# Optimization experiments

Measured on AMD Instinct MI355X. Metric: run time of the kernel, lower is better.

Reference implementation:

```python
import jax, jax.numpy as jnp
import numpy as np

B, N, NQ, D, H = 16, 1024, 1024, 512, 8
HD = D // H  # per-head kq dim and per-head v-output dim (64)


def setup_inputs() -> dict:
    key = jax.random.key(0)
    ks = jax.random.split(key, 7)
    s = 0.02  # small init like torch Linear default scale
    return {
        "x":   jax.random.normal(ks[0], (B, N, D), jnp.float32),
        "r":   jax.random.normal(ks[1], (B, N, D), jnp.float32),
        "x_q": jax.random.normal(ks[2], (B, NQ, D), jnp.float32),
        # per-head projection weights, torch Linear layout (out, in), stacked over heads
        "Wq": jax.random.normal(ks[3], (H, HD, D), jnp.float32) * s,
        "Wk": jax.random.normal(ks[4], (H, HD, D), jnp.float32) * s,
        "Wv": jax.random.normal(ks[5], (H, HD, D), jnp.float32) * s,  # applied AFTER attention
        "Wo": jax.random.normal(ks[6], (D, D), jnp.float32) * s,
    }


def reference(x, r, x_q, Wq, Wk, Wv, Wo):
    # AttentionAggregator.forward(x, r, x_q) -> MultiHeadAttention(q=x_q, k=x, v=r)
    qh = jnp.einsum('bnd,hed->bhne', x_q, Wq)            # (B,H,NQ,HD)
    kh = jnp.einsum('bmd,hed->bhme', x, Wk)              # (B,H,N,HD)
    scale = jnp.sqrt(jnp.float32(HD))                    # sqrt(d_k) with d_k = head_kq_dim_out
    scores = jnp.einsum('bhne,bhme->bhnm', qh, kh) / scale
    attn = jax.nn.softmax(scores, axis=-1)               # normalize=True path
    # NOTE: v (=r) is NOT projected before attention in the original module
    ctx = jnp.einsum('bhnm,bmd->bhnd', attn, r)          # (B,H,NQ,D)
    heads = jnp.einsum('bhnd,hed->bhne', ctx, Wv)        # (B,H,NQ,HD), per-head post-projection
    concat = heads.transpose(0, 2, 1, 3).reshape(B, NQ, H * HD)  # cat over heads, dim=-1
    return concat @ Wo.T                                 # head_o (post_process=True)
```

## Files before the change

kernel.cpp:

```cpp
#include <hip/hip_runtime.h>


#define B_  16
#define N_  1024
#define D_  512
#define H_  8

typedef short short8 __attribute__((ext_vector_type(8)));
typedef float f32x4 __attribute__((ext_vector_type(4)));
typedef unsigned short ushort;
typedef unsigned int uint;

__device__ __forceinline__ ushort bf16rne(float f) {
  uint u = __float_as_uint(f);
  u += 0x7FFFu + ((u >> 16) & 1u);
  return (ushort)(u >> 16);
}
__device__ __forceinline__ uint bf16pk(float lo, float hi) {
  return (uint)bf16rne(lo) | ((uint)bf16rne(hi) << 16);
}
__device__ __forceinline__ void gload_lds16(const void* g, void* l) {
  __builtin_amdgcn_global_load_lds(
      (const __attribute__((address_space(1))) uint*)g,
      (__attribute__((address_space(3))) uint*)l, 16, 0, 0);
}

__global__ __launch_bounds__(256) void cast_bf16_k(
    const float* __restrict__ s, ushort* __restrict__ d, long n, float scale)
{
  long i = ((long)blockIdx.x * 256 + threadIdx.x) * 8;
  if (i >= n) return;
  float4 v0 = *(const float4*)(s + i);
  float4 v1 = *(const float4*)(s + i + 4);
  uint4 o;
  o.x = bf16pk(v0.x * scale, v0.y * scale);
  o.y = bf16pk(v0.z * scale, v0.w * scale);
  o.z = bf16pk(v1.x * scale, v1.y * scale);
  o.w = bf16pk(v1.z * scale, v1.w * scale);
  *(uint4*)(d + i) = o;
}

template <typename OutT>
__global__ __launch_bounds__(256) void gemm_bt(
    const ushort* __restrict__ A, const ushort* __restrict__ W,
    OutT* __restrict__ C, int M, int N, int K)
{
  __shared__ __align__(16) ushort Al[128 * 64];
  __shared__ __align__(16) ushort Bl[128 * 64];
  const int t = threadIdx.x, lane = t & 63, w = t >> 6;
  const int g = lane >> 4, lr = lane & 15;
  const int wr = w >> 1, wc = w & 1;
  const long m0 = (long)blockIdx.y * 128, n0 = (long)blockIdx.x * 128;

  f32x4 acc[4][4] = {};

  for (int k0 = 0; k0 < K; k0 += 64) {
    __syncthreads();
    #pragma unroll
    for (int u = 0; u < 4; ++u) {
      const int a = t * 16 + u * 4096;
      const int row = a >> 7, ch = (a >> 4) & 7;
      const int kk = k0 + ((ch ^ (row & 7)) << 3);
      gload_lds16(A + (m0 + row) * K + kk, (char*)Al + a);
      gload_lds16(W + (n0 + row) * K + kk, (char*)Bl + a);
    }
    __syncthreads();

    short8 af[4][2], bf[4][2];
    #pragma unroll
    for (int mf = 0; mf < 4; ++mf)
      #pragma unroll
      for (int ks = 0; ks < 2; ++ks) {
        int row = wr * 64 + mf * 16 + lr;
        af[mf][ks] = *(const short8*)((const char*)Al + row * 128 + (((ks * 4 + g) ^ (row & 7)) << 4));
        row = wc * 64 + mf * 16 + lr;
        bf[mf][ks] = *(const short8*)((const char*)Bl + row * 128 + (((ks * 4 + g) ^ (row & 7)) << 4));
      }
    #pragma unroll
    for (int mf = 0; mf < 4; ++mf)
      #pragma unroll
      for (int nf = 0; nf < 4; ++nf)
        #pragma unroll
        for (int ks = 0; ks < 2; ++ks)
          acc[mf][nf] = __builtin_amdgcn_mfma_f32_16x16x32_bf16(
              af[mf][ks], bf[nf][ks], acc[mf][nf], 0, 0, 0);
  }

  #pragma unroll
  for (int mf = 0; mf < 4; ++mf)
    #pragma unroll
    for (int nf = 0; nf < 4; ++nf)
      #pragma unroll
      for (int r = 0; r < 4; ++r) {
        const long row = m0 + wr * 64 + mf * 16 + g * 4 + r;
        const long col = n0 + wc * 64 + nf * 16 + lr;
        const float v = acc[mf][nf][r];
        if constexpr (sizeof(OutT) == 2) ((ushort*)C)[row * N + col] = bf16rne(v);
        else                             ((float*)C)[row * N + col] = v;
      }
}

__global__ __launch_bounds__(256) void transpose_v(
    const ushort* __restrict__ Vb, ushort* __restrict__ Vt)
{
  __shared__ ushort T[64][65];
  const int t = threadIdx.x;
  const int z = blockIdx.y, b = z >> 3, h = z & 7;
  const int kt = blockIdx.x;
  #pragma unroll
  for (int u = 0; u < 2; ++u) {
    const int f = t + u * 256;
    const int kvr = f >> 3, c0 = (f & 7) * 8;
    uint4 v = *(const uint4*)(Vb + ((long)(b * N_ + kt * 64 + kvr)) * D_ + h * 64 + c0);
    const ushort* pv = (const ushort*)&v;
    #pragma unroll
    for (int j = 0; j < 8; ++j) T[c0 + j][kvr] = pv[j];
  }
  __syncthreads();
  #pragma unroll
  for (int u = 0; u < 2; ++u) {
    const int f = t + u * 256;
    const int c = f >> 3, kv0 = (f & 7) * 8;
    ushort tmp[8];
    #pragma unroll
    for (int j = 0; j < 8; ++j) tmp[j] = T[c][kv0 + j];
    *(uint4*)(Vt + ((long)z * 64 + c) * N_ + kt * 64 + kv0) = *(const uint4*)tmp;
  }
}

__global__ __launch_bounds__(256) void attn_mfma(
    const ushort* __restrict__ Q, const ushort* __restrict__ K,
    const ushort* __restrict__ Vt, ushort* __restrict__ Hd)
{
  __shared__ __align__(16) ushort Kl[64 * 64];
  __shared__ __align__(16) ushort Vl[64 * 64];
  __shared__ __align__(16) ushort Pl[4][32 * 64];
  const int t = threadIdx.x, lane = t & 63, w = t >> 6;
  const int g = lane >> 4, lr = lane & 15;
  const int z = blockIdx.y, b = z >> 3, h = z & 7;
  const int qbase = blockIdx.x * 128 + w * 32;

  short8 qf[2][2];
  #pragma unroll
  for (int nf = 0; nf < 2; ++nf)
    #pragma unroll
    for (int ks = 0; ks < 2; ++ks)
      qf[nf][ks] = *(const short8*)(Q + (long)(b * N_ + qbase + nf * 16 + lr) * D_ + h * 64 + ks * 32 + g * 8);

  f32x4 o[2][4] = {};
  float lsum[2] = {0.f, 0.f};

  const ushort* Kz = K + (long)b * N_ * D_ + h * 64;
  const ushort* Vz = Vt + (long)z * 64 * N_;
  ushort* Plw = Pl[w];

  for (int kt = 0; kt < 16; ++kt) {
    __syncthreads();
    #pragma unroll
    for (int u = 0; u < 2; ++u) {
      const int a = t * 16 + u * 4096;
      const int row = a >> 7, ch = (a >> 4) & 7;
      const int cc = (ch ^ (row & 7)) << 3;
      gload_lds16(Kz + (long)(kt * 64 + row) * D_ + cc, (char*)Kl + a);
      gload_lds16(Vz + (long)row * N_ + kt * 64 + cc, (char*)Vl + a);
    }
    __syncthreads();

    f32x4 s[4][2] = {};
    #pragma unroll
    for (int mf = 0; mf < 4; ++mf) {
      short8 kf[2];
      #pragma unroll
      for (int ks = 0; ks < 2; ++ks) {
        const int row = mf * 16 + lr;
        kf[ks] = *(const short8*)((const char*)Kl + row * 128 + (((ks * 4 + g) ^ (row & 7)) << 4));
      }
      #pragma unroll
      for (int nf = 0; nf < 2; ++nf)
        #pragma unroll
        for (int ks = 0; ks < 2; ++ks)
          s[mf][nf] = __builtin_amdgcn_mfma_f32_16x16x32_bf16(kf[ks], qf[nf][ks], s[mf][nf], 0, 0, 0);
    }

    #pragma unroll
    for (int mf = 0; mf < 4; ++mf)
      #pragma unroll
      for (int nf = 0; nf < 2; ++nf) {
        const float p0 = __expf(s[mf][nf][0]);
        const float p1 = __expf(s[mf][nf][1]);
        const float p2 = __expf(s[mf][nf][2]);
        const float p3 = __expf(s[mf][nf][3]);
        lsum[nf] += (p0 + p1) + (p2 + p3);
        const int row = nf * 16 + lr;
        const int ch = (2 * mf + (g >> 1)) ^ (row & 7);
        uint2 pk; pk.x = bf16pk(p0, p1); pk.y = bf16pk(p2, p3);
        *(uint2*)((char*)Plw + row * 128 + ch * 16 + (g & 1) * 8) = pk;
      }

    #pragma unroll
    for (int ks = 0; ks < 2; ++ks) {
      short8 pa[2], vb[4];
      #pragma unroll
      for (int mf = 0; mf < 2; ++mf) {
        const int row = mf * 16 + lr;
        pa[mf] = *(const short8*)((const char*)Plw + row * 128 + (((ks * 4 + g) ^ (row & 7)) << 4));
      }
      #pragma unroll
      for (int nf = 0; nf < 4; ++nf) {
        const int row = nf * 16 + lr;
        vb[nf] = *(const short8*)((const char*)Vl + row * 128 + (((ks * 4 + g) ^ (row & 7)) << 4));
      }
      #pragma unroll
      for (int mf = 0; mf < 2; ++mf)
        #pragma unroll
        for (int nf = 0; nf < 4; ++nf)
          o[mf][nf] = __builtin_amdgcn_mfma_f32_16x16x32_bf16(pa[mf], vb[nf], o[mf][nf], 0, 0, 0);
    }
  }

  #pragma unroll
  for (int nf = 0; nf < 2; ++nf) {
    lsum[nf] += __shfl_xor(lsum[nf], 16);
    lsum[nf] += __shfl_xor(lsum[nf], 32);
  }

  #pragma unroll
  for (int mf = 0; mf < 2; ++mf)
    #pragma unroll
    for (int r = 0; r < 4; ++r) {
      const float inv = 1.f / __shfl(lsum[mf], g * 4 + r);
      const long grow = (long)b * N_ + qbase + mf * 16 + g * 4 + r;
      #pragma unroll
      for (int nf = 0; nf < 4; ++nf)
        Hd[grow * D_ + h * 64 + nf * 16 + lr] = bf16rne(o[mf][nf][r] * inv);
    }
}

extern "C" void kernel_launch(void* const* d_in, const int* in_sizes, int n_in,
                              void* d_out, int out_size, void* d_ws, size_t ws_size,
                              hipStream_t stream) {
  const float* x   = (const float*)d_in[0];
  const float* r   = (const float*)d_in[1];
  const float* x_q = (const float*)d_in[2];
  const float* Wq  = (const float*)d_in[3];
  const float* Wk  = (const float*)d_in[4];
  const float* Wv  = (const float*)d_in[5];
  const float* Wo  = (const float*)d_in[6];

  const long SBe = (long)B_ * N_ * D_;
  const long WBe = (long)D_ * D_;
  ushort* xqb = (ushort*)d_ws;
  ushort* xb  = xqb + SBe;
  ushort* rb  = xb  + SBe;
  ushort* Qb  = rb  + SBe;
  ushort* Kb  = Qb  + SBe;
  ushort* Vb  = Kb  + SBe;
  ushort* Wqb = Vb  + SBe;
  ushort* Wkb = Wqb + WBe;
  ushort* Wvb = Wkb + WBe;
  ushort* Wob = Wvb + WBe;
  ushort* Vtb = rb;
  ushort* Hdb = xqb;

  dim3 blk(256);
  cast_bf16_k<<<4096, blk, 0, stream>>>(x_q, xqb, SBe, 1.f);
  cast_bf16_k<<<4096, blk, 0, stream>>>(x,   xb,  SBe, 1.f);
  cast_bf16_k<<<4096, blk, 0, stream>>>(r,   rb,  SBe, 1.f);
  cast_bf16_k<<<128,  blk, 0, stream>>>(Wq, Wqb, WBe, 0.125f);
  cast_bf16_k<<<128,  blk, 0, stream>>>(Wk, Wkb, WBe, 1.f);
  cast_bf16_k<<<128,  blk, 0, stream>>>(Wv, Wvb, WBe, 1.f);
  cast_bf16_k<<<128,  blk, 0, stream>>>(Wo, Wob, WBe, 1.f);

  dim3 gg(4, 128);
  gemm_bt<ushort><<<gg, blk, 0, stream>>>(xqb, Wqb, Qb, B_ * N_, D_, D_);
  gemm_bt<ushort><<<gg, blk, 0, stream>>>(xb,  Wkb, Kb, B_ * N_, D_, D_);
  gemm_bt<ushort><<<gg, blk, 0, stream>>>(rb,  Wvb, Vb, B_ * N_, D_, D_);

  transpose_v<<<dim3(16, 128), blk, 0, stream>>>(Vb, Vtb);

  attn_mfma<<<dim3(8, 128), blk, 0, stream>>>(Qb, Kb, Vtb, Hdb);

  gemm_bt<float><<<gg, blk, 0, stream>>>(Hdb, Wob, (float*)d_out, B_ * N_, D_, D_);
}
```

Measured before the change: 289.1 us.

## Batch casts and projections, fuse V transpose, double-buffer attention with register P

Merges the seven cast launches into two and the three projection GEMMs into one batched launch. The V projection now writes its output already transposed, which removes the separate transpose kernel. The attention kernel double-buffers its K/V tiles in LDS and keeps P in registers, using hardware exp2 with log2e folded into the Wq scale, pk_bf16 conversion and permlane swaps instead of an LDS round trip for P. Its grid is also reordered so that all heads of the same batch run adjacently. The costs are inline-asm dependence on gfx950 instructions, strided scattered stores for Vt, and no running max in the softmax, which the baseline also lacked.

```diff
diff --git a/kernel.cpp b/kernel.cpp
--- a/kernel.cpp
+++ b/kernel.cpp
@@ -4,7 +4,7 @@
 #define B_  16
 #define N_  1024
 #define D_  512
-#define H_  8
+#define M_  (B_ * N_)
 
 typedef short short8 __attribute__((ext_vector_type(8)));
 typedef float f32x4 __attribute__((ext_vector_type(4)));
@@ -24,27 +24,62 @@
       (const __attribute__((address_space(1))) uint*)g,
       (__attribute__((address_space(3))) uint*)l, 16, 0, 0);
 }
-
-__global__ __launch_bounds__(256) void cast_bf16_k(
-    const float* __restrict__ s, ushort* __restrict__ d, long n, float scale)
+__device__ __forceinline__ float exp2_hw(float x) {
+  float r;
+  asm("v_exp_f32 %0, %1" : "=v"(r) : "v"(x));
+  return r;
+}
+__device__ __forceinline__ uint cvtpk_bf16(float lo, float hi) {
+  uint r;
+  asm("v_cvt_pk_bf16_f32 %0, %1, %2" : "=v"(r) : "v"(lo), "v"(hi));
+  return r;
+}
+
+union U4S8 { uint u[4]; short8 s; };
+
+__global__ __launch_bounds__(256) void cast3_k(
+    const float* __restrict__ s0, const float* __restrict__ s1,
+    const float* __restrict__ s2, ushort* __restrict__ d, long n)
 {
+  const float* s = (blockIdx.y == 0) ? s0 : (blockIdx.y == 1) ? s1 : s2;
+  ushort* dz = d + (long)blockIdx.y * n;
   long i = ((long)blockIdx.x * 256 + threadIdx.x) * 8;
-  if (i >= n) return;
   float4 v0 = *(const float4*)(s + i);
   float4 v1 = *(const float4*)(s + i + 4);
   uint4 o;
-  o.x = bf16pk(v0.x * scale, v0.y * scale);
-  o.y = bf16pk(v0.z * scale, v0.w * scale);
-  o.z = bf16pk(v1.x * scale, v1.y * scale);
-  o.w = bf16pk(v1.z * scale, v1.w * scale);
-  *(uint4*)(d + i) = o;
-}
-
-template <typename OutT>
-__global__ __launch_bounds__(256) void gemm_bt(
-    const ushort* __restrict__ A, const ushort* __restrict__ W,
-    OutT* __restrict__ C, int M, int N, int K)
+  o.x = bf16pk(v0.x, v0.y); o.y = bf16pk(v0.z, v0.w);
+  o.z = bf16pk(v1.x, v1.y); o.w = bf16pk(v1.z, v1.w);
+  *(uint4*)(dz + i) = o;
+}
+
+__global__ __launch_bounds__(256) void castW_k(
+    const float* __restrict__ w0, const float* __restrict__ w1,
+    const float* __restrict__ w2, const float* __restrict__ w3,
+    ushort* __restrict__ d, long n)
 {
+  const int z = blockIdx.y;
+  const float* s = (z == 0) ? w0 : (z == 1) ? w1 : (z == 2) ? w2 : w3;
+  const float sc = (z == 0) ? 0.1803368801f : 1.f;
+  ushort* dz = d + (long)z * n;
+  long i = ((long)blockIdx.x * 256 + threadIdx.x) * 8;
+  float4 v0 = *(const float4*)(s + i);
+  float4 v1 = *(const float4*)(s + i + 4);
+  uint4 o;
+  o.x = bf16pk(v0.x * sc, v0.y * sc); o.y = bf16pk(v0.z * sc, v0.w * sc);
+  o.z = bf16pk(v1.x * sc, v1.y * sc); o.w = bf16pk(v1.z * sc, v1.w * sc);
+  *(uint4*)(dz + i) = o;
+}
+
+template <int MODE>
+__global__ __launch_bounds__(256) void gemm_k(
+    const ushort* __restrict__ Abase, const ushort* __restrict__ Wbase,
+    void* __restrict__ C0, ushort* __restrict__ Vt)
+{
+  const long SB = (long)M_ * D_, WB = (long)D_ * D_;
+  const int z = (MODE == 0) ? blockIdx.z : 0;
+  const ushort* A = Abase + z * SB;
+  const ushort* W = Wbase + z * WB;
+
   __shared__ __align__(16) ushort Al[128 * 64];
   __shared__ __align__(16) ushort Bl[128 * 64];
   const int t = threadIdx.x, lane = t & 63, w = t >> 6;
@@ -54,15 +89,15 @@
 
   f32x4 acc[4][4] = {};
 
-  for (int k0 = 0; k0 < K; k0 += 64) {
+  for (int k0 = 0; k0 < D_; k0 += 64) {
     __syncthreads();
     #pragma unroll
     for (int u = 0; u < 4; ++u) {
       const int a = t * 16 + u * 4096;
       const int row = a >> 7, ch = (a >> 4) & 7;
       const int kk = k0 + ((ch ^ (row & 7)) << 3);
-      gload_lds16(A + (m0 + row) * K + kk, (char*)Al + a);
-      gload_lds16(W + (n0 + row) * K + kk, (char*)Bl + a);
+      gload_lds16(A + (m0 + row) * D_ + kk, (char*)Al + a);
+      gload_lds16(W + (n0 + row) * D_ + kk, (char*)Bl + a);
     }
     __syncthreads();
 
@@ -86,45 +121,44 @@
               af[mf][ks], bf[nf][ks], acc[mf][nf], 0, 0, 0);
   }
 
-  #pragma unroll
-  for (int mf = 0; mf < 4; ++mf)
-    #pragma unroll
-    for (int nf = 0; nf < 4; ++nf)
-      #pragma unroll
-      for (int r = 0; r < 4; ++r) {
-        const long row = m0 + wr * 64 + mf * 16 + g * 4 + r;
-        const long col = n0 + wc * 64 + nf * 16 + lr;
-        const float v = acc[mf][nf][r];
-        if constexpr (sizeof(OutT) == 2) ((ushort*)C)[row * N + col] = bf16rne(v);
-        else                             ((float*)C)[row * N + col] = v;
-      }
-}
-
-__global__ __launch_bounds__(256) void transpose_v(
-    const ushort* __restrict__ Vb, ushort* __restrict__ Vt)
-{
-  __shared__ ushort T[64][65];
-  const int t = threadIdx.x;
-  const int z = blockIdx.y, b = z >> 3, h = z & 7;
-  const int kt = blockIdx.x;
-  #pragma unroll
-  for (int u = 0; u < 2; ++u) {
-    const int f = t + u * 256;
-    const int kvr = f >> 3, c0 = (f & 7) * 8;
-    uint4 v = *(const uint4*)(Vb + ((long)(b * N_ + kt * 64 + kvr)) * D_ + h * 64 + c0);
-    const ushort* pv = (const ushort*)&v;
-    #pragma unroll
-    for (int j = 0; j < 8; ++j) T[c0 + j][kvr] = pv[j];
-  }
-  __syncthreads();
-  #pragma unroll
-  for (int u = 0; u < 2; ++u) {
-    const int f = t + u * 256;
-    const int c = f >> 3, kv0 = (f & 7) * 8;
-    ushort tmp[8];
-    #pragma unroll
-    for (int j = 0; j < 8; ++j) tmp[j] = T[c][kv0 + j];
-    *(uint4*)(Vt + ((long)z * 64 + c) * N_ + kt * 64 + kv0) = *(const uint4*)tmp;
+  if constexpr (MODE == 1) {
+    float* C = (float*)C0;
+    #pragma unroll
+    for (int mf = 0; mf < 4; ++mf)
+      #pragma unroll
+      for (int nf = 0; nf < 4; ++nf)
+        #pragma unroll
+        for (int r = 0; r < 4; ++r)
+          C[(m0 + wr * 64 + mf * 16 + g * 4 + r) * D_ + n0 + wc * 64 + nf * 16 + lr] =
+              acc[mf][nf][r];
+  } else {
+    if (z < 2) {
+      ushort* C = (ushort*)C0 + z * SB;
+      #pragma unroll
+      for (int mf = 0; mf < 4; ++mf)
+        #pragma unroll
+        for (int nf = 0; nf < 4; ++nf)
+          #pragma unroll
+          for (int r = 0; r < 4; ++r)
+            C[(m0 + wr * 64 + mf * 16 + g * 4 + r) * D_ + n0 + wc * 64 + nf * 16 + lr] =
+                bf16rne(acc[mf][nf][r]);
+    } else {
+      const int hh = (int)(n0 >> 6) + wc;
+      #pragma unroll
+      for (int mf = 0; mf < 4; ++mf) {
+        const long m = m0 + wr * 64 + mf * 16 + g * 4;
+        const int bb = (int)(m >> 10);
+        const int kv = (int)(m & 1023);
+        #pragma unroll
+        for (int nf = 0; nf < 4; ++nf) {
+          const int c = nf * 16 + lr;
+          ushort4 o4;
+          o4.x = bf16rne(acc[mf][nf][0]); o4.y = bf16rne(acc[mf][nf][1]);
+          o4.z = bf16rne(acc[mf][nf][2]); o4.w = bf16rne(acc[mf][nf][3]);
+          *(ushort4*)&Vt[((long)(bb * 8 + hh) * 64 + c) * (long)N_ + kv] = o4;
+        }
+      }
+    }
   }
 }
 
@@ -132,13 +166,13 @@
     const ushort* __restrict__ Q, const ushort* __restrict__ K,
     const ushort* __restrict__ Vt, ushort* __restrict__ Hd)
 {
-  __shared__ __align__(16) ushort Kl[64 * 64];
-  __shared__ __align__(16) ushort Vl[64 * 64];
-  __shared__ __align__(16) ushort Pl[4][32 * 64];
+  __shared__ __align__(16) ushort Kl[2][64 * 64];
+  __shared__ __align__(16) ushort Vl[2][64 * 64];
   const int t = threadIdx.x, lane = t & 63, w = t >> 6;
   const int g = lane >> 4, lr = lane & 15;
-  const int z = blockIdx.y, b = z >> 3, h = z & 7;
-  const int qbase = blockIdx.x * 128 + w * 32;
+  const int bid = blockIdx.x;
+  const int z = bid & 127, b = z >> 3, h = z & 7;
+  const int qbase = (bid >> 7) * 128 + w * 32;
 
   short8 qf[2][2];
   #pragma unroll
@@ -152,19 +186,24 @@
 
   const ushort* Kz = K + (long)b * N_ * D_ + h * 64;
   const ushort* Vz = Vt + (long)z * 64 * N_;
-  ushort* Plw = Pl[w];
-
-  for (int kt = 0; kt < 16; ++kt) {
-    __syncthreads();
+
+  auto STAGE = [&](int kt, int bufi) {
     #pragma unroll
     for (int u = 0; u < 2; ++u) {
       const int a = t * 16 + u * 4096;
       const int row = a >> 7, ch = (a >> 4) & 7;
       const int cc = (ch ^ (row & 7)) << 3;
-      gload_lds16(Kz + (long)(kt * 64 + row) * D_ + cc, (char*)Kl + a);
-      gload_lds16(Vz + (long)row * N_ + kt * 64 + cc, (char*)Vl + a);
-    }
-    __syncthreads();
+      gload_lds16(Kz + (long)(kt * 64 + row) * D_ + cc, (char*)Kl[bufi] + a);
+      gload_lds16(Vz + (long)row * N_ + kt * 64 + cc, (char*)Vl[bufi] + a);
+    }
+  };
+
+  STAGE(0, 0);
+  __syncthreads();
+
+  for (int kt = 0; kt < 16; ++kt) {
+    const int cur = kt & 1;
+    if (kt < 15) STAGE(kt + 1, cur ^ 1);
 
     f32x4 s[4][2] = {};
     #pragma unroll
@@ -173,7 +212,7 @@
       #pragma unroll
       for (int ks = 0; ks < 2; ++ks) {
         const int row = mf * 16 + lr;
-        kf[ks] = *(const short8*)((const char*)Kl + row * 128 + (((ks * 4 + g) ^ (row & 7)) << 4));
+        kf[ks] = *(const short8*)((const char*)Kl[cur] + row * 128 + (((ks * 4 + g) ^ (row & 7)) << 4));
       }
       #pragma unroll
       for (int nf = 0; nf < 2; ++nf)
@@ -182,40 +221,50 @@
           s[mf][nf] = __builtin_amdgcn_mfma_f32_16x16x32_bf16(kf[ks], qf[nf][ks], s[mf][nf], 0, 0, 0);
     }
 
-    #pragma unroll
-    for (int mf = 0; mf < 4; ++mf)
-      #pragma unroll
-      for (int nf = 0; nf < 2; ++nf) {
-        const float p0 = __expf(s[mf][nf][0]);
-        const float p1 = __expf(s[mf][nf][1]);
-        const float p2 = __expf(s[mf][nf][2]);
-        const float p3 = __expf(s[mf][nf][3]);
-        lsum[nf] += (p0 + p1) + (p2 + p3);
-        const int row = nf * 16 + lr;
-        const int ch = (2 * mf + (g >> 1)) ^ (row & 7);
-        uint2 pk; pk.x = bf16pk(p0, p1); pk.y = bf16pk(p2, p3);
-        *(uint2*)((char*)Plw + row * 128 + ch * 16 + (g & 1) * 8) = pk;
-      }
+    short8 pa[2][2];
+    #pragma unroll
+    for (int nf = 0; nf < 2; ++nf) {
+      uint Apk[4], Bpk[4];
+      #pragma unroll
+      for (int mf = 0; mf < 4; ++mf) {
+        const float e0 = exp2_hw(s[mf][nf][0]);
+        const float e1 = exp2_hw(s[mf][nf][1]);
+        const float e2 = exp2_hw(s[mf][nf][2]);
+        const float e3 = exp2_hw(s[mf][nf][3]);
+        lsum[nf] += (e0 + e1) + (e2 + e3);
+        Apk[mf] = cvtpk_bf16(e0, e1);
+        Bpk[mf] = cvtpk_bf16(e2, e3);
+      }
+      asm("v_permlane32_swap_b32 %0, %1" : "+v"(Apk[0]), "+v"(Apk[1]));
+      asm("v_permlane16_swap_b32 %0, %1" : "+v"(Apk[0]), "+v"(Apk[1]));
+      asm("v_permlane32_swap_b32 %0, %1" : "+v"(Bpk[0]), "+v"(Bpk[1]));
+      asm("v_permlane16_swap_b32 %0, %1" : "+v"(Bpk[0]), "+v"(Bpk[1]));
+      asm("v_permlane32_swap_b32 %0, %1" : "+v"(Apk[2]), "+v"(Apk[3]));
+      asm("v_permlane16_swap_b32 %0, %1" : "+v"(Apk[2]), "+v"(Apk[3]));
+      asm("v_permlane32_swap_b32 %0, %1" : "+v"(Bpk[2]), "+v"(Bpk[3]));
+      asm("v_permlane16_swap_b32 %0, %1" : "+v"(Bpk[2]), "+v"(Bpk[3]));
+      U4S8 u0, u1;
+      u0.u[0] = Apk[0]; u0.u[1] = Bpk[0]; u0.u[2] = Apk[1]; u0.u[3] = Bpk[1];
+      u1.u[0] = Apk[2]; u1.u[1] = Bpk[2]; u1.u[2] = Apk[3]; u1.u[3] = Bpk[3];
+      pa[nf][0] = u0.s;
+      pa[nf][1] = u1.s;
+    }
 
     #pragma unroll
     for (int ks = 0; ks < 2; ++ks) {
-      short8 pa[2], vb[4];
-      #pragma unroll
-      for (int mf = 0; mf < 2; ++mf) {
-        const int row = mf * 16 + lr;
-        pa[mf] = *(const short8*)((const char*)Plw + row * 128 + (((ks * 4 + g) ^ (row & 7)) << 4));
-      }
+      short8 vb[4];
       #pragma unroll
       for (int nf = 0; nf < 4; ++nf) {
         const int row = nf * 16 + lr;
-        vb[nf] = *(const short8*)((const char*)Vl + row * 128 + (((ks * 4 + g) ^ (row & 7)) << 4));
+        vb[nf] = *(const short8*)((const char*)Vl[cur] + row * 128 + (((ks * 4 + g) ^ (row & 7)) << 4));
       }
       #pragma unroll
       for (int mf = 0; mf < 2; ++mf)
         #pragma unroll
         for (int nf = 0; nf < 4; ++nf)
-          o[mf][nf] = __builtin_amdgcn_mfma_f32_16x16x32_bf16(pa[mf], vb[nf], o[mf][nf], 0, 0, 0);
-    }
+          o[mf][nf] = __builtin_amdgcn_mfma_f32_16x16x32_bf16(pa[mf][ks], vb[nf], o[mf][nf], 0, 0, 0);
+    }
+    __syncthreads();
   }
 
   #pragma unroll
@@ -247,38 +296,24 @@
   const float* Wv  = (const float*)d_in[5];
   const float* Wo  = (const float*)d_in[6];
 
-  const long SBe = (long)B_ * N_ * D_;
+  const long SBe = (long)M_ * D_;
   const long WBe = (long)D_ * D_;
   ushort* xqb = (ushort*)d_ws;
   ushort* xb  = xqb + SBe;
   ushort* rb  = xb  + SBe;
   ushort* Qb  = rb  + SBe;
   ushort* Kb  = Qb  + SBe;
-  ushort* Vb  = Kb  + SBe;
-  ushort* Wqb = Vb  + SBe;
-  ushort* Wkb = Wqb + WBe;
-  ushort* Wvb = Wkb + WBe;
-  ushort* Wob = Wvb + WBe;
-  ushort* Vtb = rb;
+  ushort* Vtb = Kb  + SBe;
+  ushort* Wqb = Vtb + SBe;
   ushort* Hdb = xqb;
 
   dim3 blk(256);
-  cast_bf16_k<<<4096, blk, 0, stream>>>(x_q, xqb, SBe, 1.f);
-  cast_bf16_k<<<4096, blk, 0, stream>>>(x,   xb,  SBe, 1.f);
-  cast_bf16_k<<<4096, blk, 0, stream>>>(r,   rb,  SBe, 1.f);
-  cast_bf16_k<<<128,  blk, 0, stream>>>(Wq, Wqb, WBe, 0.125f);
-  cast_bf16_k<<<128,  blk, 0, stream>>>(Wk, Wkb, WBe, 1.f);
-  cast_bf16_k<<<128,  blk, 0, stream>>>(Wv, Wvb, WBe, 1.f);
-  cast_bf16_k<<<128,  blk, 0, stream>>>(Wo, Wob, WBe, 1.f);
-
-  dim3 gg(4, 128);
-  gemm_bt<ushort><<<gg, blk, 0, stream>>>(xqb, Wqb, Qb, B_ * N_, D_, D_);
-  gemm_bt<ushort><<<gg, blk, 0, stream>>>(xb,  Wkb, Kb, B_ * N_, D_, D_);
-  gemm_bt<ushort><<<gg, blk, 0, stream>>>(rb,  Wvb, Vb, B_ * N_, D_, D_);
-
-  transpose_v<<<dim3(16, 128), blk, 0, stream>>>(Vb, Vtb);
-
-  attn_mfma<<<dim3(8, 128), blk, 0, stream>>>(Qb, Kb, Vtb, Hdb);
-
-  gemm_bt<float><<<gg, blk, 0, stream>>>(Hdb, Wob, (float*)d_out, B_ * N_, D_, D_);
-}
+  cast3_k<<<dim3(4096, 3), blk, 0, stream>>>(x_q, x, r, xqb, SBe);
+  castW_k<<<dim3(128, 4),  blk, 0, stream>>>(Wq, Wk, Wv, Wo, Wqb, WBe);
+
+  gemm_k<0><<<dim3(4, 128, 3), blk, 0, stream>>>(xqb, Wqb, Qb, Vtb);
+
+  attn_mfma<<<dim3(1024), blk, 0, stream>>>(Qb, Kb, Vtb, Hdb);
+
+  gemm_k<1><<<dim3(4, 128), blk, 0, stream>>>(Hdb, Wqb + 3 * WBe, d_out, nullptr);
+}
```

After: 269.1 us. 1.07x faster.
